# Kernel optimization log

Measured on AMD Instinct MI355X. Metric: run time of the kernel, lower is better.

The kernel has to match this reference:

```python
import jax, jax.numpy as jnp
import numpy as np

N_NODES = 50000
N_EDGES = 800000
IN_DIM = 128
HID_DIM = 128
NUM_GRAPHS = 64


def gcn_conv(x, edge_index, W, b):
    """PyG GCNConv: symmetric-normalized aggregation with self-loops.
    out = D^{-1/2} (A + I) D^{-1/2} (x @ W) + b
    """
    n = x.shape[0]
    loop = jnp.arange(n, dtype=edge_index.dtype)
    src = jnp.concatenate([edge_index[0], loop])  # [E+N]
    dst = jnp.concatenate([edge_index[1], loop])
    deg = jax.ops.segment_sum(jnp.ones_like(dst, x.dtype), dst, num_segments=n)
    dinv = jnp.where(deg > 0, jax.lax.rsqrt(deg), 0.0)
    norm = dinv[src] * dinv[dst]  # [E+N]
    h = x @ W  # [N, H] transform before propagate (PyG order)
    msg = h[src] * norm[:, None]  # [E+N, H] gathered+scaled messages
    out = jax.ops.segment_sum(msg, dst, num_segments=n)  # scatter-add
    return out + b


def global_mean_pool(x, batch, num_graphs):
    s = jax.ops.segment_sum(x, batch, num_segments=num_graphs)
    cnt = jax.ops.segment_sum(jnp.ones((x.shape[0],), x.dtype), batch, num_segments=num_graphs)
    return s / jnp.maximum(cnt, 1.0)[:, None]


def setup_inputs() -> dict:
    key = jax.random.key(0)
    ks = jax.random.split(key, 8)
    x = jax.random.normal(ks[0], (N_NODES, IN_DIM), dtype=jnp.float32)
    edge_index = jax.random.randint(ks[1], (2, N_EDGES), 0, N_NODES, dtype=jnp.int64)
    batch = jnp.sort(jax.random.randint(ks[2], (N_NODES,), 0, NUM_GRAPHS, dtype=jnp.int64))
    s1 = 1.0 / np.sqrt(IN_DIM)
    s2 = 1.0 / np.sqrt(HID_DIM)
    W1 = jax.random.uniform(ks[3], (IN_DIM, HID_DIM), jnp.float32, -s1, s1)
    b1 = jnp.zeros((HID_DIM,), jnp.float32)
    W2 = jax.random.uniform(ks[4], (HID_DIM, HID_DIM), jnp.float32, -s2, s2)
    b2 = jnp.zeros((HID_DIM,), jnp.float32)
    Wc = jax.random.uniform(ks[5], (HID_DIM, 1), jnp.float32, -s2, s2)
    bc = jnp.zeros((1,), jnp.float32)
    return {"x": x, "edge_index": edge_index, "batch": batch,
            "W1": W1, "b1": b1, "W2": W2, "b2": b2, "Wc": Wc, "bc": bc}


def reference(x, edge_index, batch, W1, b1, W2, b2, Wc, bc):
    h = jax.nn.relu(gcn_conv(x, edge_index, W1, b1))
    # dropout p=0.1 is identity in eval mode
    h = gcn_conv(h, edge_index, W2, b2)
    g = global_mean_pool(h, batch, NUM_GRAPHS)  # [G, H]
    return jax.nn.sigmoid(g @ Wc + bc)  # [G, 1]
```

## Files before the change

kernel.cpp:

```cpp
#include <hip/hip_runtime.h>
#include <hip/hip_bf16.h>
#include <hip/hip_fp16.h>

#define N_NODES 50000
#define N_EDGES 800000
#define DIM     128
#define NG      64
#define GN      16
#define CAP     48
#define AGG_EB  512
#define LAXP    136

#define NBIN    196
#define SORT_B  500
#define EPB     1600
#define SROUND  7

#define CAST_B  1563
#define VB_B    129
#define WF_B    8

typedef float  f2_t  __attribute__((ext_vector_type(2)));
typedef float  f32x4 __attribute__((ext_vector_type(4)));
typedef _Float16 f16x8 __attribute__((ext_vector_type(8)));
typedef _Float16 f16x4 __attribute__((ext_vector_type(4)));

__global__ void k_prep(const int* __restrict__ ei, int* __restrict__ binCnt,
                       int* __restrict__ blockHist,
                       const float* __restrict__ W2, const float* __restrict__ Wc,
                       const float* __restrict__ b2, float* __restrict__ v,
                       float* __restrict__ beta2,
                       const float* __restrict__ W1, f16x8* __restrict__ w1f) {
    __shared__ float red[4];
    __shared__ int hist[256];
    int bid = blockIdx.x, t = threadIdx.x;
    if (bid < SORT_B) {
        hist[t] = 0;
        __syncthreads();
        int base = bid * EPB;
        for (int r = 0; r < SROUND; r++) {
            int idx = r * 256 + t;
            if (idx < EPB) {
                int d = ei[N_EDGES + base + idx];
                atomicAdd(&hist[d >> 8], 1);
            }
        }
        __syncthreads();
        if (t < NBIN) {
            blockHist[bid * 256 + t] = hist[t];
            if (hist[t] > 0) atomicAdd(&binCnt[t], hist[t]);
        }
    } else if (bid < SORT_B + VB_B) {
        int b = bid - SORT_B;
        float p = 0.f;
        if (t < DIM) p = (b < DIM) ? W2[b * DIM + t] * Wc[t] : b2[t] * Wc[t];
        #pragma unroll
        for (int off = 32; off > 0; off >>= 1) p += __shfl_down(p, off, 64);
        if ((t & 63) == 0) red[t >> 6] = p;
        __syncthreads();
        if (t == 0) {
            float s = red[0] + red[1];
            if (b < DIM) v[b] = s; else beta2[0] = s;
        }
    } else {
        int idx = (bid - (SORT_B + VB_B)) * 256 + t;
        int ntile = idx >> 8, kb = (idx >> 6) & 3, l = idx & 63;
        int kbase = kb * 32 + (l >> 4) * 8;
        int n = ntile * 16 + (l & 15);
        f16x8 o;
        #pragma unroll
        for (int j = 0; j < 8; j++) o[j] = (_Float16)W1[(kbase + j) * DIM + n];
        w1f[idx] = o;
    }
}

__global__ void k_scatter(const int* __restrict__ ei, const int* __restrict__ binCnt,
                          const int* __restrict__ blockHist,
                          int* __restrict__ binCur, int* __restrict__ binOff,
                          unsigned int* __restrict__ sorted) {
    __shared__ int soff[256];
    __shared__ int cur[256];
    int bid = blockIdx.x, t = threadIdx.x;
    int c = (t < NBIN) ? binCnt[t] : 0;
    soff[t] = c;
    #pragma unroll
    for (int o = 1; o < 256; o <<= 1) {
        __syncthreads();
        int v2 = (t >= o) ? soff[t - o] : 0;
        __syncthreads();
        soff[t] += v2;
    }
    __syncthreads();
    int excl = soff[t] - c;
    if (bid == 0 && t < NBIN) binOff[t] = excl;
    int myh = (t < NBIN) ? blockHist[bid * 256 + t] : 0;
    if (myh > 0) cur[t] = excl + atomicAdd(&binCur[t], myh);
    __syncthreads();
    int base = bid * EPB;
    for (int r = 0; r < SROUND; r++) {
        int idx = r * 256 + t;
        if (idx < EPB) {
            int e = base + idx;
            int s = ei[e];
            int d = ei[N_EDGES + e];
            int pos = atomicAdd(&cur[d >> 8], 1);
            sorted[pos] = (unsigned)s | ((unsigned)(d & 255) << 16);
        }
    }
}

__global__ __launch_bounds__(512) void k_csr(const unsigned int* __restrict__ sorted,
                      const int* __restrict__ binOff, int* __restrict__ deg,
                      unsigned short* __restrict__ csr) {
    __shared__ int cur[256];
    int b = blockIdx.x, t = threadIdx.x;
    if (t < 256) cur[t] = 0;
    __syncthreads();
    int lo = binOff[b];
    int hi = (b == NBIN - 1) ? N_EDGES : binOff[b + 1];
    for (int i = lo + t; i < hi; i += 512) {
        unsigned e = sorted[i];
        unsigned src = e & 0xFFFFu;
        unsigned dLow = e >> 16;
        int pos = atomicAdd(&cur[dLow], 1);
        if (pos < CAP) csr[(size_t)(b * 256 + dLow) * CAP + pos] = (unsigned short)src;
    }
    __syncthreads();
    int node = b * 256 + t;
    if (t < 256 && node < N_NODES) deg[node] = cur[t];
}

__global__ void k_cast(const float4* __restrict__ x4, uint4* __restrict__ xq4,
                       const int* __restrict__ deg, const int* __restrict__ batch,
                       unsigned int* __restrict__ bd) {
    int idx = blockIdx.x * 256 + threadIdx.x;
    if (idx >= (N_NODES + 1) * 8) return;
    if (idx >= N_NODES * 8) {
        xq4[idx] = make_uint4(0u, 0u, 0u, 0u);
        return;
    }
    int node = idx >> 3;
    float di = rsqrtf((float)deg[node] + 1.f);
    uint4 o;
    unsigned* op = (unsigned*)&o;
    #pragma unroll
    for (int q = 0; q < 4; q++) {
        float4 f = x4[idx * 4 + q];
        int p = 0;
        p = __builtin_amdgcn_cvt_pk_fp8_f32(di * f.x, di * f.y, p, false);
        p = __builtin_amdgcn_cvt_pk_fp8_f32(di * f.z, di * f.w, p, true);
        op[q] = (unsigned)p;
    }
    xq4[idx] = o;
    if ((idx & 7) == 0) {
        unsigned hw = (unsigned)__half_as_ushort(__float2half(di));
        bd[node] = ((unsigned)batch[node] & 0xFFFFu) | (hw << 16);
    }
}

__global__ __launch_bounds__(512) void k_node(
    const unsigned int* __restrict__ xq,
    const unsigned short* __restrict__ csr,
    const f16x8* __restrict__ w1f,
    const float* __restrict__ b1,
    const float* __restrict__ v, const int* __restrict__ deg,
    float* __restrict__ z2) {
    __shared__ _Float16 laxh[GN * LAXP];
    __shared__ float redm[GN * 8];
    int tid = threadIdx.x;
    int w = tid >> 6, l = tid & 63;
    int half = l >> 5, hl = l & 31;
    int node0 = blockIdx.x * GN;

    {
        int i = node0 + 2 * w + half;
        int dg = deg[i];
        int len = min(dg, CAP);
        float di = rsqrtf((float)dg + 1.f);

        unsigned su = xq[(size_t)i * 32 + hl];
        f2_t s01 = __builtin_amdgcn_cvt_pk_f32_fp8((int)su, false);
        f2_t s23 = __builtin_amdgcn_cvt_pk_f32_fp8((int)su, true);
        float ax[8], ay[8], az[8], aw[8];
        #pragma unroll
        for (int k = 0; k < 8; k++) { ax[k] = 0.f; ay[k] = 0.f; az[k] = 0.f; aw[k] = 0.f; }
        ax[0] = s01.x; ay[0] = s01.y;
        az[0] = s23.x; aw[0] = s23.y;

        int lenmax = max(len, __shfl_xor(len, 32, 64));
        int lmp = (lenmax + 7) & ~7;
        const uint4* csr4 = (const uint4*)(csr + (size_t)i * CAP);
        for (int j = 0; j < lmp; j += 8) {
            uint4 cw = csr4[j >> 3];
            unsigned cw8[4] = {cw.x, cw.y, cw.z, cw.w};
            unsigned q[8];
            #pragma unroll
            for (int k = 0; k < 8; k++) {
                unsigned id = (cw8[k >> 1] >> ((k & 1) * 16)) & 0xFFFFu;
                unsigned idc = (j + k < len) ? id : (unsigned)N_NODES;
                q[k] = xq[(size_t)idc * 32 + hl];
            }
            #pragma unroll
            for (int k = 0; k < 8; k++) {
                f2_t e01 = __builtin_amdgcn_cvt_pk_f32_fp8((int)q[k], false);
                f2_t e23 = __builtin_amdgcn_cvt_pk_f32_fp8((int)q[k], true);
                ax[k] += e01.x; ay[k] += e01.y;
                az[k] += e23.x; aw[k] += e23.y;
            }
        }
        float a0 = 0.f, a1 = 0.f, a2 = 0.f, a3 = 0.f;
        #pragma unroll
        for (int k = 0; k < 8; k++) { a0 += ax[k]; a1 += ay[k]; a2 += az[k]; a3 += aw[k]; }
        f16x4 pk;
        pk[0] = (_Float16)(di * a0); pk[1] = (_Float16)(di * a1);
        pk[2] = (_Float16)(di * a2); pk[3] = (_Float16)(di * a3);
        *(f16x4*)&laxh[(2 * w + half) * LAXP + 4 * hl] = pk;
    }
    __syncthreads();

    f32x4 acc = {0.f, 0.f, 0.f, 0.f};
    #pragma unroll
    for (int kb = 0; kb < 4; kb++) {
        f16x8 af = *(const f16x8*)&laxh[(l & 15) * LAXP + kb * 32 + (l >> 4) * 8];
        f16x8 bf = w1f[(w * 4 + kb) * 64 + l];
        acc = __builtin_amdgcn_mfma_f32_16x16x32_f16(af, bf, acc, 0, 0, 0);
    }
    int n = w * 16 + (l & 15);
    float bn = b1[n], vn = v[n];
    #pragma unroll
    for (int r = 0; r < 4; r++) {
        float p = fmaxf(acc[r] + bn, 0.f) * vn;
        p += __shfl_xor(p, 1, 64);
        p += __shfl_xor(p, 2, 64);
        p += __shfl_xor(p, 4, 64);
        p += __shfl_xor(p, 8, 64);
        if ((l & 15) == 0) redm[((l >> 4) * 4 + r) * 8 + w] = p;
    }
    __syncthreads();
    if (tid < GN) {
        float s = 0.f;
        #pragma unroll
        for (int q = 0; q < 8; q++) s += redm[tid * 8 + q];
        z2[node0 + tid] = rsqrtf((float)deg[node0 + tid] + 1.f) * s;
    }
}

__global__ void k_aggz(const float* __restrict__ z2, const unsigned int* __restrict__ bd,
                       const int* __restrict__ ei, const int* __restrict__ batch,
                       float* __restrict__ gpartE, float* __restrict__ gpartN,
                       int* __restrict__ gcnt) {
    int bid = blockIdx.x, t = threadIdx.x;
    if (bid < AGG_EB) {
        __shared__ float bs[4][NG];
        bs[t >> 6][t & 63] = 0.f;
        __syncthreads();
        int wg = t >> 6;
        for (int base = bid * 1024; base < N_EDGES; base += AGG_EB * 1024) {
            #pragma unroll
            for (int k = 0; k < 4; k++) {
                int e = base + k * 256 + t;
                if (e < N_EDGES) {
                    int s = ei[e];
                    int d = ei[N_EDGES + e];
                    unsigned u = bd[d];
                    float dv = __half2float(__ushort_as_half((unsigned short)(u >> 16)));
                    atomicAdd(&bs[wg][u & 63u], dv * z2[s]);
                }
            }
        }
        __syncthreads();
        if (t < NG) gpartE[bid * NG + t] = bs[0][t] + bs[1][t] + bs[2][t] + bs[3][t];
    } else {
        __shared__ int range[2];
        __shared__ float rs[4];
        int g = bid - AGG_EB;
        if (t < 2) {
            int key = g + t;
            int lo = 0, hi = N_NODES;
            while (lo < hi) { int m = (lo + hi) >> 1; if (batch[m] < key) lo = m + 1; else hi = m; }
            range[t] = lo;
        }
        __syncthreads();
        int lo = range[0], hi = range[1];
        float loc = 0.f;
        for (int i = lo + t; i < hi; i += 256)
            loc += __half2float(__ushort_as_half((unsigned short)(bd[i] >> 16))) * z2[i];
        #pragma unroll
        for (int off = 32; off > 0; off >>= 1) loc += __shfl_down(loc, off, 64);
        if ((t & 63) == 0) rs[t >> 6] = loc;
        __syncthreads();
        if (t == 0) {
            gpartN[g] = rs[0] + rs[1] + rs[2] + rs[3];
            gcnt[g] = hi - lo;
        }
    }
}

__global__ void k_final(const float* __restrict__ gpartE, const float* __restrict__ gpartN,
                        const int* __restrict__ gcnt, const float* __restrict__ beta2,
                        const float* __restrict__ bcin, float* __restrict__ out) {
    __shared__ float acc[4][NG];
    int t = threadIdx.x;
    int g = t & 63, c = t >> 6;
    float s = 0.f;
    for (int k = 0; k < AGG_EB / 4; k++)
        s += gpartE[(c * (AGG_EB / 4) + k) * NG + g];
    acc[c][g] = s;
    __syncthreads();
    if (t < NG) {
        float tot = acc[0][t] + acc[1][t] + acc[2][t] + acc[3][t] + gpartN[t];
        int cnt = gcnt[t];
        float val = tot / (float)(cnt > 0 ? cnt : 1) + beta2[0] + bcin[0];
        out[t] = 1.f / (1.f + expf(-val));
    }
}

extern "C" void kernel_launch(void* const* d_in, const int* in_sizes, int n_in,
                              void* d_out, int out_size, void* d_ws, size_t ws_size,
                              hipStream_t stream) {
    const float* x   = (const float*)d_in[0];
    const int*   ei  = (const int*)  d_in[1];
    const int*   bat = (const int*)  d_in[2];
    const float* W1  = (const float*)d_in[3];
    const float* b1  = (const float*)d_in[4];
    const float* W2  = (const float*)d_in[5];
    const float* b2  = (const float*)d_in[6];
    const float* Wc  = (const float*)d_in[7];
    const float* bc  = (const float*)d_in[8];
    float* out = (float*)d_out;

    char* w = (char*)d_ws;
    size_t off = 0;
    auto alloc = [&](size_t bytes) -> void* {
        void* p = w + off;
        off = (off + bytes + 255) & ~(size_t)255;
        return p;
    };
    int*   binCnt  = (int*)  alloc(NBIN * 4);
    int*   binCur  = (int*)  alloc(NBIN * 4);
    size_t zero_len = off;
    int*   binOff  = (int*)  alloc(NBIN * 4);
    int*   deg     = (int*)  alloc(N_NODES * 4);
    float* z2      = (float*)alloc(N_NODES * 4);
    float* v       = (float*)alloc(DIM * 4);
    float* beta2   = (float*)alloc(4);
    float* gpartE  = (float*)alloc((size_t)AGG_EB * NG * 4);
    float* gpartN  = (float*)alloc(NG * 4);
    int*   gcnt    = (int*)  alloc(NG * 4);
    unsigned int* bd = (unsigned int*)alloc(N_NODES * 4);
    f16x8* w1f     = (f16x8*)alloc(2048 * 16);
    int*   blockHist = (int*)alloc((size_t)SORT_B * 256 * 4);
    unsigned int* xq = (unsigned int*)alloc((size_t)(N_NODES + 1) * DIM);
    unsigned int* sorted = (unsigned int*)alloc((size_t)N_EDGES * 4);
    unsigned short* csr = (unsigned short*)alloc((size_t)N_NODES * CAP * 2);
    (void)ws_size; (void)in_sizes; (void)n_in; (void)out_size;

    hipMemsetAsync(d_ws, 0, zero_len, stream);

    dim3 b256(256);
    k_prep<<<dim3(SORT_B + VB_B + WF_B), b256, 0, stream>>>(
        ei, binCnt, blockHist, W2, Wc, b2, v, beta2, W1, w1f);
    k_scatter<<<dim3(SORT_B), b256, 0, stream>>>(
        ei, binCnt, blockHist, binCur, binOff, sorted);
    k_csr<<<dim3(NBIN), dim3(512), 0, stream>>>(sorted, binOff, deg, csr);
    k_cast<<<dim3(CAST_B), b256, 0, stream>>>(
        (const float4*)x, (uint4*)xq, deg, bat, bd);
    k_node<<<dim3(N_NODES / GN), dim3(512), 0, stream>>>(
        xq, csr, w1f, b1, v, deg, z2);
    k_aggz<<<dim3(AGG_EB + NG), b256, 0, stream>>>(
        z2, bd, ei, bat, gpartE, gpartN, gcnt);
    k_final<<<dim3(1), b256, 0, stream>>>(gpartE, gpartN, gcnt, beta2, bc, out);
}
```

Measured before the change: 174.8 us.

## Remove memset and final launch via deterministic prefix sums and last-block ticket

Replaces the global atomic bin counters with a per-block prefix over the stored block histograms, so the workspace memset is no longer needed. Fuses the final reduction into the aggregation kernel through a last-block-done ticket counter, which k_csr resets. It also halves the sort and aggregation block counts and doubles k_csr's block size. These changes remove two stream operations, at the cost of a serial 250-iteration histogram scan in every scatter block and less parallelism in the sort and aggregation kernels.

```diff
diff --git a/kernel.cpp b/kernel.cpp
--- a/kernel.cpp
+++ b/kernel.cpp
@@ -8,13 +8,13 @@
 #define NG      64
 #define GN      16
 #define CAP     48
-#define AGG_EB  512
+#define AGG_EB  256
 #define LAXP    136
 
 #define NBIN    196
-#define SORT_B  500
-#define EPB     1600
-#define SROUND  7
+#define SORT_B  250
+#define EPB     3200
+#define SROUND  13
 
 #define CAST_B  1563
 #define VB_B    129
@@ -25,8 +25,7 @@
 typedef _Float16 f16x8 __attribute__((ext_vector_type(8)));
 typedef _Float16 f16x4 __attribute__((ext_vector_type(4)));
 
-__global__ void k_prep(const int* __restrict__ ei, int* __restrict__ binCnt,
-                       int* __restrict__ blockHist,
+__global__ void k_prep(const int* __restrict__ ei, int* __restrict__ blockHist,
                        const float* __restrict__ W2, const float* __restrict__ Wc,
                        const float* __restrict__ b2, float* __restrict__ v,
                        float* __restrict__ beta2,
@@ -46,10 +45,7 @@
             }
         }
         __syncthreads();
-        if (t < NBIN) {
-            blockHist[bid * 256 + t] = hist[t];
-            if (hist[t] > 0) atomicAdd(&binCnt[t], hist[t]);
-        }
+        if (t < NBIN) blockHist[bid * 256 + t] = hist[t];
     } else if (bid < SORT_B + VB_B) {
         int b = bid - SORT_B;
         float p = 0.f;
@@ -74,14 +70,19 @@
     }
 }
 
-__global__ void k_scatter(const int* __restrict__ ei, const int* __restrict__ binCnt,
-                          const int* __restrict__ blockHist,
-                          int* __restrict__ binCur, int* __restrict__ binOff,
-                          unsigned int* __restrict__ sorted) {
+__global__ void k_scatter(const int* __restrict__ ei, const int* __restrict__ blockHist,
+                          int* __restrict__ binOff, unsigned int* __restrict__ sorted) {
     __shared__ int soff[256];
     __shared__ int cur[256];
     int bid = blockIdx.x, t = threadIdx.x;
-    int c = (t < NBIN) ? binCnt[t] : 0;
+    int c = 0, pre = 0;
+    if (t < NBIN) {
+        for (int b = 0; b < SORT_B; b++) {
+            int h = blockHist[b * 256 + t];
+            c += h;
+            pre += (b < bid) ? h : 0;
+        }
+    }
     soff[t] = c;
     #pragma unroll
     for (int o = 1; o < 256; o <<= 1) {
@@ -93,8 +94,7 @@
     __syncthreads();
     int excl = soff[t] - c;
     if (bid == 0 && t < NBIN) binOff[t] = excl;
-    int myh = (t < NBIN) ? blockHist[bid * 256 + t] : 0;
-    if (myh > 0) cur[t] = excl + atomicAdd(&binCur[t], myh);
+    if (t < NBIN) cur[t] = excl + pre;
     __syncthreads();
     int base = bid * EPB;
     for (int r = 0; r < SROUND; r++) {
@@ -109,16 +109,16 @@
     }
 }
 
-__global__ __launch_bounds__(512) void k_csr(const unsigned int* __restrict__ sorted,
+__global__ __launch_bounds__(1024) void k_csr(const unsigned int* __restrict__ sorted,
                       const int* __restrict__ binOff, int* __restrict__ deg,
-                      unsigned short* __restrict__ csr) {
+                      unsigned short* __restrict__ csr, int* __restrict__ ticket) {
     __shared__ int cur[256];
     int b = blockIdx.x, t = threadIdx.x;
     if (t < 256) cur[t] = 0;
     __syncthreads();
     int lo = binOff[b];
     int hi = (b == NBIN - 1) ? N_EDGES : binOff[b + 1];
-    for (int i = lo + t; i < hi; i += 512) {
+    for (int i = lo + t; i < hi; i += 1024) {
         unsigned e = sorted[i];
         unsigned src = e & 0xFFFFu;
         unsigned dLow = e >> 16;
@@ -128,6 +128,7 @@
     __syncthreads();
     int node = b * 256 + t;
     if (t < 256 && node < N_NODES) deg[node] = cur[t];
+    if (b == 0 && t == 300) *ticket = 0;
 }
 
 __global__ void k_cast(const float4* __restrict__ x4, uint4* __restrict__ xq4,
@@ -248,10 +249,15 @@
 __global__ void k_aggz(const float* __restrict__ z2, const unsigned int* __restrict__ bd,
                        const int* __restrict__ ei, const int* __restrict__ batch,
                        float* __restrict__ gpartE, float* __restrict__ gpartN,
-                       int* __restrict__ gcnt) {
+                       int* __restrict__ gcnt, int* __restrict__ ticket,
+                       const float* __restrict__ beta2, const float* __restrict__ bcin,
+                       float* __restrict__ out) {
+    __shared__ float bs[4][NG];
+    __shared__ int range[2];
+    __shared__ float rs[4];
+    __shared__ int isLast;
     int bid = blockIdx.x, t = threadIdx.x;
     if (bid < AGG_EB) {
-        __shared__ float bs[4][NG];
         bs[t >> 6][t & 63] = 0.f;
         __syncthreads();
         int wg = t >> 6;
@@ -271,8 +277,6 @@
         __syncthreads();
         if (t < NG) gpartE[bid * NG + t] = bs[0][t] + bs[1][t] + bs[2][t] + bs[3][t];
     } else {
-        __shared__ int range[2];
-        __shared__ float rs[4];
         int g = bid - AGG_EB;
         if (t < 2) {
             int key = g + t;
@@ -294,24 +298,24 @@
             gcnt[g] = hi - lo;
         }
     }
-}
-
-__global__ void k_final(const float* __restrict__ gpartE, const float* __restrict__ gpartN,
-                        const int* __restrict__ gcnt, const float* __restrict__ beta2,
-                        const float* __restrict__ bcin, float* __restrict__ out) {
-    __shared__ float acc[4][NG];
-    int t = threadIdx.x;
-    int g = t & 63, c = t >> 6;
-    float s = 0.f;
-    for (int k = 0; k < AGG_EB / 4; k++)
-        s += gpartE[(c * (AGG_EB / 4) + k) * NG + g];
-    acc[c][g] = s;
-    __syncthreads();
-    if (t < NG) {
-        float tot = acc[0][t] + acc[1][t] + acc[2][t] + acc[3][t] + gpartN[t];
-        int cnt = gcnt[t];
-        float val = tot / (float)(cnt > 0 ? cnt : 1) + beta2[0] + bcin[0];
-        out[t] = 1.f / (1.f + expf(-val));
+    __threadfence();
+    if (t == 0) isLast = (atomicAdd(ticket, 1) == AGG_EB + NG - 1) ? 1 : 0;
+    __syncthreads();
+    if (isLast) {
+        __threadfence();
+        int g = t & 63, c = t >> 6;
+        float s = 0.f;
+        for (int k = 0; k < AGG_EB / 4; k++)
+            s += gpartE[(c * (AGG_EB / 4) + k) * NG + g];
+        __syncthreads();
+        bs[c][g] = s;
+        __syncthreads();
+        if (t < NG) {
+            float tot = bs[0][t] + bs[1][t] + bs[2][t] + bs[3][t] + gpartN[t];
+            int cnt = gcnt[t];
+            float val = tot / (float)(cnt > 0 ? cnt : 1) + beta2[0] + bcin[0];
+            out[t] = 1.f / (1.f + expf(-val));
+        }
     }
 }
 
@@ -336,9 +340,6 @@
         off = (off + bytes + 255) & ~(size_t)255;
         return p;
     };
-    int*   binCnt  = (int*)  alloc(NBIN * 4);
-    int*   binCur  = (int*)  alloc(NBIN * 4);
-    size_t zero_len = off;
     int*   binOff  = (int*)  alloc(NBIN * 4);
     int*   deg     = (int*)  alloc(N_NODES * 4);
     float* z2      = (float*)alloc(N_NODES * 4);
@@ -347,6 +348,7 @@
     float* gpartE  = (float*)alloc((size_t)AGG_EB * NG * 4);
     float* gpartN  = (float*)alloc(NG * 4);
     int*   gcnt    = (int*)  alloc(NG * 4);
+    int*   ticket  = (int*)  alloc(4);
     unsigned int* bd = (unsigned int*)alloc(N_NODES * 4);
     f16x8* w1f     = (f16x8*)alloc(2048 * 16);
     int*   blockHist = (int*)alloc((size_t)SORT_B * 256 * 4);
@@ -355,19 +357,16 @@
     unsigned short* csr = (unsigned short*)alloc((size_t)N_NODES * CAP * 2);
     (void)ws_size; (void)in_sizes; (void)n_in; (void)out_size;
 
-    hipMemsetAsync(d_ws, 0, zero_len, stream);
-
     dim3 b256(256);
     k_prep<<<dim3(SORT_B + VB_B + WF_B), b256, 0, stream>>>(
-        ei, binCnt, blockHist, W2, Wc, b2, v, beta2, W1, w1f);
+        ei, blockHist, W2, Wc, b2, v, beta2, W1, w1f);
     k_scatter<<<dim3(SORT_B), b256, 0, stream>>>(
-        ei, binCnt, blockHist, binCur, binOff, sorted);
-    k_csr<<<dim3(NBIN), dim3(512), 0, stream>>>(sorted, binOff, deg, csr);
+        ei, blockHist, binOff, sorted);
+    k_csr<<<dim3(NBIN), dim3(1024), 0, stream>>>(sorted, binOff, deg, csr, ticket);
     k_cast<<<dim3(CAST_B), b256, 0, stream>>>(
         (const float4*)x, (uint4*)xq, deg, bat, bd);
     k_node<<<dim3(N_NODES / GN), dim3(512), 0, stream>>>(
         xq, csr, w1f, b1, v, deg, z2);
     k_aggz<<<dim3(AGG_EB + NG), b256, 0, stream>>>(
-        z2, bd, ei, bat, gpartE, gpartN, gcnt);
-    k_final<<<dim3(1), b256, 0, stream>>>(gpartE, gpartN, gcnt, beta2, bc, out);
-}
+        z2, bd, ei, bat, gpartE, gpartN, gcnt, ticket, beta2, bc, out);
+}
```

New measurement: 186.8 us. +6.8%, slower.
